# Kernel tuning notes

Measured on AMD Instinct MI355X. Metric: run time of the kernel, lower is better.

## Reference

```python
import jax, jax.numpy as jnp
import numpy as np

L = 5  # number of attention+MLP stages

def _layernorm(x, g, b, eps=1e-5):
    mu = x.mean(-1, keepdims=True)
    var = ((x - mu) ** 2).mean(-1, keepdims=True)
    return (x - mu) * jax.lax.rsqrt(var + eps) * g + b

def setup_inputs() -> dict:
    key = jax.random.key(0)
    B, N, C = 8, 2048, 512  # win_size=4, num_slices=12 -> C = 4*4*384//12 = 512
    ks = jax.random.split(key, 7)
    s = 0.02
    return {
        "x": jax.random.normal(ks[0], (B, N, C), dtype=jnp.float32),
        "qkv_w": jax.random.normal(ks[1], (L, C, 3 * C), dtype=jnp.float32) * s,
        "qkv_b": jnp.zeros((L, 3 * C), dtype=jnp.float32),
        "ln_g": jnp.ones((L, C), dtype=jnp.float32),
        "ln_b": jnp.zeros((L, C), dtype=jnp.float32),
        "fc1_w": jax.random.normal(ks[2], (L, C, 2 * C), dtype=jnp.float32) * s,
        "fc1_b": jnp.zeros((L, 2 * C), dtype=jnp.float32),
        "fc2_w": jax.random.normal(ks[3], (L, 2 * C, C), dtype=jnp.float32) * s,
        "fc2_b": jnp.zeros((L, C), dtype=jnp.float32),
    }

def reference(x, qkv_w, qkv_b, ln_g, ln_b, fc1_w, fc1_b, fc2_w, fc2_b):
    B, N, C = x.shape
    half = N // 2
    scale = C ** -0.5  # num_heads = 1 -> head_dim = C
    # Custom block mask: top-left (half x half) block fully visible,
    # top-right block masked; bottom half is tril with diagonal = N//2,
    # i.e. global row i >= half may attend to columns j <= i.
    i = jnp.arange(N)[:, None]
    j = jnp.arange(N)[None, :]
    allowed = jnp.where(i < half, j < half, j <= i)
    bias = jnp.where(allowed, 0.0, -1000.0).astype(x.dtype)  # (N, N)
    for l in range(L):
        # Mask3dAttention (single head)
        qkv = x @ qkv_w[l] + qkv_b[l]                      # (B, N, 3C)
        q, k, v = jnp.split(qkv, 3, axis=-1)               # each (B, N, C)
        attn = jnp.einsum("bnc,bmc->bnm", q * scale, k) + bias
        attn = jax.nn.softmax(attn, axis=-1)
        x = jnp.einsum("bnm,bmc->bnc", attn, v)
        # residual MLP on normed features
        y = _layernorm(x, ln_g[l], ln_b[l])
        h = jax.nn.gelu(y @ fc1_w[l] + fc1_b[l], approximate=False)
        x = x + (h @ fc2_w[l] + fc2_b[l])
    return x
```

## Files before the change

### kernel.cpp

```cpp
#include <hip/hip_runtime.h>
#include <math.h>

typedef unsigned short u16;
typedef __attribute__((ext_vector_type(8))) short bf16x8;
typedef __attribute__((ext_vector_type(4))) float f32x4;
typedef __attribute__((ext_vector_type(4))) unsigned short u16x4;

#define NLAYERS 5
#define BATCH 8
#define SEQ 2048
#define CH 512
#define ROWS_TOTAL (BATCH * SEQ)
#define HALF (SEQ / 2)
#define QSCALE_EXP2 0.06375871529f
#define EXP2_CAP 86.56f

#define SMEM_U16 32768
#define QK2_U16 32768

__device__ __forceinline__ u16 f2bf(float f) {
    unsigned u = __float_as_uint(f);
    u += 0x7fffu + ((u >> 16) & 1u);
    return (u16)(u >> 16);
}

__device__ __forceinline__ unsigned pk2(float a, float b) {
    unsigned r;
    asm("v_cvt_pk_bf16_f32 %0, %1, %2" : "=v"(r) : "v"(a), "v"(b));
    return r;
}

__device__ __forceinline__ u16x4 pack4(f32x4 v) {
    union { unsigned u[2]; u16x4 o; } r;
    r.u[0] = pk2(v[0], v[1]);
    r.u[1] = pk2(v[2], v[3]);
    return r.o;
}

__device__ __forceinline__ void st16(u16* p, u16x4 v) { *(u16x4*)p = v; }
__device__ __forceinline__ void st16f(float* p, f32x4 v) { *(f32x4*)p = v; }

__device__ __forceinline__ float fexp2(float x) {
    float r;
    asm("v_exp_f32 %0, %1" : "=v"(r) : "v"(x));
    return r;
}

__device__ __forceinline__ void llds16(const u16* g, u16* l) {
    __builtin_amdgcn_global_load_lds(
        (const __attribute__((address_space(1))) unsigned int*)g,
        (__attribute__((address_space(3))) unsigned int*)l, 16, 0, 0);
}

__device__ __forceinline__ void xcd_rc(int& rt, int& ct) {
    const int n = blockIdx.x;
    const int m = n >> 3;
    rt = (n & 7) * 16 + (m & 15);
    ct = m >> 4;
}

__device__ __forceinline__ void mm_compute(const u16* As, const u16* Bs,
                                           const int aoff[2][4],
                                           const int boff[2][4],
                                           f32x4 acc[4][4])
{
#pragma unroll
    for (int h = 0; h < 2; ++h) {
        bf16x8 af[4], bfv[4];
#pragma unroll
        for (int t = 0; t < 4; ++t) af[t]  = *(const bf16x8*)&As[aoff[h][t]];
#pragma unroll
        for (int t = 0; t < 4; ++t) bfv[t] = *(const bf16x8*)&Bs[boff[h][t]];
#pragma unroll
        for (int ti = 0; ti < 4; ++ti)
#pragma unroll
            for (int tj = 0; tj < 4; ++tj)
                acc[ti][tj] = __builtin_amdgcn_mfma_f32_16x16x32_bf16(
                    af[ti], bfv[tj], acc[ti][tj], 0, 0, 0);
    }
}

__device__ __forceinline__ void mm_issue(const u16* gA, const u16* gB,
                                         u16* lA, u16* lB, int lda, int ldb)
{
#pragma unroll
    for (int i = 0; i < 4; ++i)
        llds16(gA + (size_t)i * 32 * lda, lA + i * 2048);
#pragma unroll
    for (int i = 0; i < 4; ++i)
        llds16(gB + (size_t)i * 32 * ldb, lB + i * 2048);
}

__device__ __forceinline__ void mm_core(
    const u16* __restrict__ A, int lda,
    const u16* __restrict__ Bt, int ldb,
    int row0, int col0, int K,
    u16* SM, f32x4 acc[4][4])
{
    const int tid  = threadIdx.x;
    const int wave = tid >> 6, lane = tid & 63;
    const int wm = (wave & 1) * 64, wn = (wave >> 1) * 64;
    const int q  = lane >> 4,  ln = lane & 15;

    const int sr8 = lane >> 3;
    const int sc  = (lane & 7) ^ sr8;
    const u16* gA = A  + (size_t)(row0 + wave * 8 + sr8) * lda + sc * 8;
    const u16* gB = Bt + (size_t)(col0 + wave * 8 + sr8) * ldb + sc * 8;

    u16* const A0 = SM;
    u16* const B0 = SM + 8192;
    u16* const A1 = SM + 16384;
    u16* const B1 = SM + 24576;
    u16* const w0a = A0 + wave * 512;
    u16* const w0b = B0 + wave * 512;
    u16* const w1a = A1 + wave * 512;
    u16* const w1b = B1 + wave * 512;

    int aoff[2][4], boff[2][4];
#pragma unroll
    for (int h = 0; h < 2; ++h) {
        const int pos = (((h * 4 + q) ^ (ln & 7)) * 8);
#pragma unroll
        for (int t = 0; t < 4; ++t) {
            aoff[h][t] = (wm + t * 16 + ln) * 64 + pos;
            boff[h][t] = (wn + t * 16 + ln) * 64 + pos;
        }
    }

#pragma unroll
    for (int ti = 0; ti < 4; ++ti)
#pragma unroll
        for (int tj = 0; tj < 4; ++tj)
#pragma unroll
            for (int e = 0; e < 4; ++e) acc[ti][tj][e] = 0.f;

    mm_issue(gA, gB, w0a, w0b, lda, ldb);
    gA += 64; gB += 64;

    for (int k0 = 0; k0 < K; k0 += 128) {
        if (k0 + 64 < K) {
            mm_issue(gA, gB, w1a, w1b, lda, ldb);
            gA += 64; gB += 64;
            asm volatile("s_waitcnt vmcnt(8)" ::: "memory");
        } else {
            asm volatile("s_waitcnt vmcnt(0)" ::: "memory");
        }
        __builtin_amdgcn_s_barrier();
        mm_compute(A0, B0, aoff, boff, acc);
        __builtin_amdgcn_s_barrier();
        __builtin_amdgcn_sched_barrier(0);
        if (k0 + 128 < K) {
            mm_issue(gA, gB, w0a, w0b, lda, ldb);
            gA += 64; gB += 64;
            asm volatile("s_waitcnt vmcnt(8)" ::: "memory");
        } else {
            asm volatile("s_waitcnt vmcnt(0)" ::: "memory");
        }
        __builtin_amdgcn_s_barrier();
        mm_compute(A1, B1, aoff, boff, acc);
        __builtin_amdgcn_s_barrier();
        __builtin_amdgcn_sched_barrier(0);
    }
}

template <typename F>
__device__ __forceinline__ void epi_emit(f32x4 acc[4][4], float* eb, F emit)
{
    const int tid = threadIdx.x, wave = tid >> 6, lane = tid & 63;
    const int wn = (wave >> 1) * 64;
    const int q = lane >> 4, ln = lane & 15;
#pragma unroll
    for (int p = 0; p < 4; ++p) {
        __syncthreads();
        if ((wave & 1) == (p >> 1)) {
            const int tibase = (p & 1) * 2;
#pragma unroll
            for (int tj = 0; tj < 4; ++tj)
#pragma unroll
                for (int t2 = 0; t2 < 2; ++t2)
#pragma unroll
                    for (int r = 0; r < 4; ++r)
                        eb[(t2 * 16 + q * 4 + r) * 132 + wn + tj * 16 + ln] =
                            acc[tibase + t2][tj][r];
        }
        __syncthreads();
#pragma unroll
        for (int s = 0; s < 4; ++s) {
            const int row = s * 8 + (tid >> 5);
            const int col = (tid & 31) * 4;
            f32x4 v = *(const f32x4*)&eb[row * 132 + col];
            emit(p * 32 + row, col, v);
        }
    }
}

__global__ __launch_bounds__(256) void qkv_gemm(
    const u16* __restrict__ A, const u16* __restrict__ Bt,
    const float* __restrict__ bias,
    u16* __restrict__ Qb, u16* __restrict__ Kb, u16* __restrict__ Vt,
    float* __restrict__ rowsum)
{
    __shared__ __align__(16) u16 SMEM[SMEM_U16];
    f32x4 acc[4][4];
    int rt, ct; xcd_rc(rt, ct);
    const int row0 = rt * 128, col0 = ct * 128;
    if (ct == 0 && threadIdx.x < 128)
        rowsum[row0 + threadIdx.x] = 0.f;
    mm_core(A, CH, Bt, CH, row0, col0, CH, SMEM, acc);

    if (ct < 8) {
        u16* dst = (ct < 4) ? Qb : Kb;
        const int cbase = (ct < 4) ? col0 : col0 - CH;
        const float sc = (ct < 4) ? QSCALE_EXP2 : 1.0f;
        epi_emit(acc, (float*)SMEM, [&](int row, int col, f32x4 v) {
            const float4 bb = *(const float4*)&bias[col0 + col];
            v[0] = (v[0] + bb.x) * sc; v[1] = (v[1] + bb.y) * sc;
            v[2] = (v[2] + bb.z) * sc; v[3] = (v[3] + bb.w) * sc;
            st16(&dst[(size_t)(row0 + row) * CH + cbase + col], pack4(v));
        });
    } else {
        const int tid = threadIdx.x, wave = tid >> 6, lane = tid & 63;
        const int wm = (wave & 1) * 64, wn = (wave >> 1) * 64;
        const int q = lane >> 4, ln = lane & 15;
#pragma unroll
        for (int tj = 0; tj < 4; ++tj) {
            const int gcol = col0 + wn + tj * 16 + ln;
            const float bv = bias[gcol];
#pragma unroll
            for (int ti = 0; ti < 4; ++ti) {
                const int grow = row0 + wm + ti * 16 + q * 4;
                const int b = grow >> 11, j = grow & (SEQ - 1);
                f32x4 vv;
                vv[0] = acc[ti][tj][0] + bv; vv[1] = acc[ti][tj][1] + bv;
                vv[2] = acc[ti][tj][2] + bv; vv[3] = acc[ti][tj][3] + bv;
                st16(&Vt[(size_t)b * CH * SEQ +
                         (size_t)(gcol - 2 * CH) * SEQ + j], pack4(vv));
            }
        }
    }
}

__global__ __launch_bounds__(512, 4) void qk2_gemm(
    const u16* __restrict__ Qb, const u16* __restrict__ Kb,
    u16* __restrict__ Sb, float* __restrict__ rowsum)
{
    __shared__ __align__(16) u16 SMEM[QK2_U16];
    u16* const B0 = SMEM;
    u16* const B1 = SMEM + 16384;
    float* const eb = (float*)SMEM;

    const int id = blockIdx.x;
    const int b = id & 7;
    int u = id >> 3, it, pr;
    if (u < 32) { it = u >> 2; pr = u & 3; }
    else {
        int v = u - 32; it = 8; int len = 5;
        while (v >= len) { v -= len; ++it; len = 5 + ((it - 8) >> 1); }
        pr = v;
    }

    const int tid = threadIdx.x;
    const int w = tid >> 6, lane = tid & 63;
    const int wq = w & 3;
    const int wm = (wq & 1) * 64;
    const int wn = (w >> 2) * 128 + (wq >> 1) * 64;
    const int q = lane >> 4, ln = lane & 15;
    const int sr8 = lane >> 3, sc = (lane & 7) ^ sr8;

    const int row0 = it * 128, col0 = pr * 256;
    const u16* const Qg = Qb + (size_t)b * SEQ * CH;
    const u16* const Kg = Kb + (size_t)b * SEQ * CH;
    u16* const S = Sb + (size_t)b * SEQ * SEQ;

    const u16* gB = Kg + (size_t)(col0 + w * 32 + sr8) * CH + sc * 8;
    u16* const lB0 = B0 + w * 2048;
    u16* const lB1 = B1 + w * 2048;

    const u16* const gAf = Qg + (size_t)(row0 + wm + ln) * CH + q * 8;

    int boff[2][4];
#pragma unroll
    for (int h = 0; h < 2; ++h) {
        const int pos = (((h * 4 + q) ^ (ln & 7)) * 8);
#pragma unroll
        for (int t = 0; t < 4; ++t)
            boff[h][t] = (wn + t * 16 + ln) * 64 + pos;
    }

    f32x4 acc[4][4];
#pragma unroll
    for (int ti = 0; ti < 4; ++ti)
#pragma unroll
        for (int tj = 0; tj < 4; ++tj)
#pragma unroll
            for (int e = 0; e < 4; ++e) acc[ti][tj][e] = 0.f;

#pragma unroll
    for (int i = 0; i < 4; ++i)
        llds16(gB + (size_t)(i * 8) * CH, lB0 + i * 512);

    for (int s = 0; s < 8; ++s) {
        bf16x8 af[2][4];
#pragma unroll
        for (int h = 0; h < 2; ++h)
#pragma unroll
            for (int t = 0; t < 4; ++t)
                af[h][t] = *(const bf16x8*)(gAf + (size_t)(t * 16) * CH
                                            + s * 64 + h * 32);
        if (s < 7) {
            u16* const nb = (s & 1) ? lB0 : lB1;
#pragma unroll
            for (int i = 0; i < 4; ++i)
                llds16(gB + (size_t)(i * 8) * CH + (s + 1) * 64, nb + i * 512);
            asm volatile("s_waitcnt vmcnt(4)" ::: "memory");
        } else {
            asm volatile("s_waitcnt vmcnt(0)" ::: "memory");
        }
        __builtin_amdgcn_s_barrier();
        const u16* const Bc = (s & 1) ? B1 : B0;
#pragma unroll
        for (int h = 0; h < 2; ++h) {
            bf16x8 bfv[4];
#pragma unroll
            for (int t = 0; t < 4; ++t)
                bfv[t] = *(const bf16x8*)&Bc[boff[h][t]];
#pragma unroll
            for (int ti = 0; ti < 4; ++ti)
#pragma unroll
                for (int tj = 0; tj < 4; ++tj)
                    acc[ti][tj] = __builtin_amdgcn_mfma_f32_16x16x32_bf16(
                        af[h][ti], bfv[tj], acc[ti][tj], 0, 0, 0);
        }
        __builtin_amdgcn_s_barrier();
        __builtin_amdgcn_sched_barrier(0);
    }

    const bool upper = (it < 8);
#pragma unroll
    for (int p = 0; p < 4; ++p) {
        __syncthreads();
        if ((wq & 1) == (p >> 1)) {
            const int tibase = (p & 1) * 2;
#pragma unroll
            for (int tj = 0; tj < 4; ++tj)
#pragma unroll
                for (int t2 = 0; t2 < 2; ++t2)
#pragma unroll
                    for (int r = 0; r < 4; ++r)
                        eb[(t2 * 16 + q * 4 + r) * 260 + wn + tj * 16 + ln] =
                            acc[tibase + t2][tj][r];
        }
        __syncthreads();
#pragma unroll
        for (int s2 = 0; s2 < 4; ++s2) {
            const int row = s2 * 8 + w;
            const int col = lane * 4;
            f32x4 v = *(const f32x4*)&eb[row * 260 + col];
            const int grow = row0 + p * 32 + row;
            const int gcol = col0 + col;
            f32x4 pv;
#pragma unroll
            for (int e = 0; e < 4; ++e) {
                const bool allowed = upper || (gcol + e <= grow);
                pv[e] = allowed ? fexp2(fminf(v[e], EXP2_CAP)) : 0.f;
            }
            st16(&S[(size_t)grow * SEQ + gcol], pack4(pv));
            float rs = pv[0] + pv[1] + pv[2] + pv[3];
            rs += __shfl_xor(rs, 1, 64);
            rs += __shfl_xor(rs, 2, 64);
            rs += __shfl_xor(rs, 4, 64);
            rs += __shfl_xor(rs, 8, 64);
            rs += __shfl_xor(rs, 16, 64);
            rs += __shfl_xor(rs, 32, 64);
            if (lane == 0)
                atomicAdd(&rowsum[b * SEQ + grow], rs);
        }
    }
}

__global__ __launch_bounds__(256) void pv_gemm(
    const u16* __restrict__ Sb, const u16* __restrict__ Vt,
    const float* __restrict__ rowsum, float* __restrict__ O)
{
    const int n = blockIdx.x;
    const int b = n & 7, m = n >> 3;
    const int it = 15 - (m >> 2), ct = m & 3;
    const int Kfull = ((it < 8) ? 8 : (it + 1)) * 128;
    __shared__ __align__(16) u16 SMEM[SMEM_U16];
    f32x4 acc[4][4];
    const u16* A  = Sb + (size_t)b * SEQ * SEQ;
    const u16* Bt = Vt + (size_t)b * CH * SEQ;
    const int row0 = it * 128, col0 = ct * 128;
    mm_core(A, SEQ, Bt, SEQ, row0, col0, Kfull, SMEM, acc);

    epi_emit(acc, (float*)SMEM, [&](int row, int col, f32x4 v) {
        const int grow = row0 + row;
        const float rden = 1.0f / rowsum[b * SEQ + grow];
        v[0] *= rden; v[1] *= rden; v[2] *= rden; v[3] *= rden;
        st16f(&O[(size_t)(b * SEQ + grow) * CH + col0 + col], v);
    });
}

__global__ __launch_bounds__(256) void fc1_gemm(
    const u16* __restrict__ A, const u16* __restrict__ Bt,
    const float* __restrict__ bias, u16* __restrict__ H)
{
    __shared__ __align__(16) u16 SMEM[SMEM_U16];
    f32x4 acc[4][4];
    int rt, ct; xcd_rc(rt, ct);
    const int row0 = rt * 128, col0 = ct * 128;
    mm_core(A, CH, Bt, CH, row0, col0, CH, SMEM, acc);
    epi_emit(acc, (float*)SMEM, [&](int row, int col, f32x4 v) {
        const float4 bb = *(const float4*)&bias[col0 + col];
        v[0] += bb.x; v[1] += bb.y; v[2] += bb.z; v[3] += bb.w;
#pragma unroll
        for (int e = 0; e < 4; ++e)
            v[e] = 0.5f * v[e] * (1.f + erff(v[e] * 0.70710678118654752f));
        st16(&H[(size_t)(row0 + row) * (2 * CH) + col0 + col], pack4(v));
    });
}

template <bool WRITE_X>
__global__ __launch_bounds__(256) void fc2_gemm(
    const u16* __restrict__ A, const u16* __restrict__ Bt,
    const float* __restrict__ bias, float* __restrict__ X,
    u16* __restrict__ Xb)
{
    __shared__ __align__(16) u16 SMEM[SMEM_U16];
    f32x4 acc[4][4];
    int rt, ct; xcd_rc(rt, ct);
    const int row0 = rt * 128, col0 = ct * 128;
    mm_core(A, 2 * CH, Bt, 2 * CH, row0, col0, 2 * CH, SMEM, acc);
    epi_emit(acc, (float*)SMEM, [&](int row, int col, f32x4 v) {
        const size_t idx = (size_t)(row0 + row) * CH + col0 + col;
        const float4 bb = *(const float4*)&bias[col0 + col];
        const f32x4 xv = *(const f32x4*)&X[idx];
        v[0] += bb.x + xv[0]; v[1] += bb.y + xv[1];
        v[2] += bb.z + xv[2]; v[3] += bb.w + xv[3];
        if (WRITE_X) st16f(&X[idx], v);
        st16(&Xb[idx], pack4(v));
    });
}

__global__ __launch_bounds__(256) void ln_kernel(
    const float* __restrict__ x, const float* __restrict__ g,
    const float* __restrict__ bta, u16* __restrict__ y)
{
    const int tid = threadIdx.x, wave = tid >> 6, lane = tid & 63;
    const int row = (blockIdx.x & 7) * SEQ + (blockIdx.x >> 3) * 4 + wave;
    const size_t base = (size_t)row * CH + lane * 8;
    const float4 a = *(const float4*)&x[base];
    const float4 b = *(const float4*)&x[base + 4];
    float s = a.x + a.y + a.z + a.w + b.x + b.y + b.z + b.w;
#pragma unroll
    for (int off = 1; off < 64; off <<= 1) s += __shfl_xor(s, off, 64);
    const float mu = s * (1.f / CH);
    float d[8] = { a.x - mu, a.y - mu, a.z - mu, a.w - mu,
                   b.x - mu, b.y - mu, b.z - mu, b.w - mu };
    float ss = 0.f;
#pragma unroll
    for (int e = 0; e < 8; ++e) ss += d[e] * d[e];
#pragma unroll
    for (int off = 1; off < 64; off <<= 1) ss += __shfl_xor(ss, off, 64);
    const float w = 1.f / sqrtf(ss * (1.f / CH) + 1e-5f);
    const int c = lane * 8;
    const float4 g0 = *(const float4*)&g[c],   g1 = *(const float4*)&g[c + 4];
    const float4 t0 = *(const float4*)&bta[c], t1 = *(const float4*)&bta[c + 4];
    uint4 o;
    o.x = pk2(d[0] * w * g0.x + t0.x, d[1] * w * g0.y + t0.y);
    o.y = pk2(d[2] * w * g0.z + t0.z, d[3] * w * g0.w + t0.w);
    o.z = pk2(d[4] * w * g1.x + t1.x, d[5] * w * g1.y + t1.y);
    o.w = pk2(d[6] * w * g1.z + t1.z, d[7] * w * g1.w + t1.w);
    *(uint4*)&y[base] = o;
}

__global__ __launch_bounds__(256) void f2bf_kernel(
    const float* __restrict__ in, u16* __restrict__ out)
{
    const int i = blockIdx.x * 256 + threadIdx.x;
    float4 vv = ((const float4*)in)[i];
    f32x4 v; v[0] = vv.x; v[1] = vv.y; v[2] = vv.z; v[3] = vv.w;
    u16x4 o = pack4(v);
    *(u16x4*)&out[(size_t)i * 4] = o;
}

__global__ __launch_bounds__(256) void wtrans_kernel(
    const float* __restrict__ in, u16* __restrict__ out, int K, int N)
{
    __shared__ float tile[32][33];
    const int l = blockIdx.z;
    in  += (size_t)l * K * N;
    out += (size_t)l * K * N;
    const int n0 = blockIdx.x * 32, k0 = blockIdx.y * 32;
    const int r = threadIdx.x >> 3, c4 = (threadIdx.x & 7) * 4;
    float4 v = *(const float4*)&in[(size_t)(k0 + r) * N + n0 + c4];
    tile[r][c4 + 0] = v.x; tile[r][c4 + 1] = v.y;
    tile[r][c4 + 2] = v.z; tile[r][c4 + 3] = v.w;
    __syncthreads();
    f32x4 t;
    t[0] = tile[c4 + 0][r]; t[1] = tile[c4 + 1][r];
    t[2] = tile[c4 + 2][r]; t[3] = tile[c4 + 3][r];
    st16(&out[(size_t)(n0 + r) * K + k0 + c4], pack4(t));
}

extern "C" void kernel_launch(void* const* d_in, const int* in_sizes, int n_in,
                              void* d_out, int out_size, void* d_ws, size_t ws_size,
                              hipStream_t stream)
{
    const float* x_in  = (const float*)d_in[0];
    const float* qkv_w = (const float*)d_in[1];
    const float* qkv_b = (const float*)d_in[2];
    const float* ln_g  = (const float*)d_in[3];
    const float* ln_b  = (const float*)d_in[4];
    const float* fc1_w = (const float*)d_in[5];
    const float* fc1_b = (const float*)d_in[6];
    const float* fc2_w = (const float*)d_in[7];
    const float* fc2_b = (const float*)d_in[8];

    float* xbuf = (float*)d_out;

    char* p = (char*)d_ws;
    u16* qkv_wt = (u16*)p; p += (size_t)NLAYERS * 1536 * 512 * 2;
    u16* fc1_wt = (u16*)p; p += (size_t)NLAYERS * 1024 * 512 * 2;
    u16* fc2_wt = (u16*)p; p += (size_t)NLAYERS * 512 * 1024 * 2;
    u16* xb = (u16*)p; p += (size_t)ROWS_TOTAL * CH * 2;
    u16* Qb = (u16*)p; p += (size_t)ROWS_TOTAL * CH * 2;
    u16* Kb = (u16*)p; p += (size_t)ROWS_TOTAL * CH * 2;
    u16* Vt = (u16*)p; p += (size_t)ROWS_TOTAL * CH * 2;
    float* rowsum = (float*)p; p += (size_t)ROWS_TOTAL * 4;
    u16* Sb = (u16*)p;
    u16* yb = Sb;
    u16* hb = Sb + (size_t)ROWS_TOTAL * CH;

    const dim3 blk(256);
    const dim3 blk2(512);

    f2bf_kernel<<<dim3(ROWS_TOTAL * CH / 1024), blk, 0, stream>>>(x_in, xb);
    wtrans_kernel<<<dim3(1536 / 32, 512 / 32, NLAYERS), blk, 0, stream>>>(
        qkv_w, qkv_wt, 512, 1536);
    wtrans_kernel<<<dim3(1024 / 32, 512 / 32, NLAYERS), blk, 0, stream>>>(
        fc1_w, fc1_wt, 512, 1024);
    wtrans_kernel<<<dim3(512 / 32, 1024 / 32, NLAYERS), blk, 0, stream>>>(
        fc2_w, fc2_wt, 1024, 512);

    for (int l = 0; l < NLAYERS; ++l) {
        qkv_gemm<<<dim3(128 * 12), blk, 0, stream>>>(
            xb, qkv_wt + (size_t)l * 1536 * 512, qkv_b + (size_t)l * 1536,
            Qb, Kb, Vt, rowsum);
        qk2_gemm<<<dim3(672), blk2, 0, stream>>>(Qb, Kb, Sb, rowsum);
        pv_gemm<<<dim3(512), blk, 0, stream>>>(Sb, Vt, rowsum, xbuf);
        ln_kernel<<<dim3(ROWS_TOTAL / 4), blk, 0, stream>>>(
            xbuf, ln_g + (size_t)l * CH, ln_b + (size_t)l * CH, yb);
        fc1_gemm<<<dim3(128 * 8), blk, 0, stream>>>(
            yb, fc1_wt + (size_t)l * 1024 * 512, fc1_b + (size_t)l * 1024, hb);
        if (l < NLAYERS - 1)
            fc2_gemm<false><<<dim3(128 * 4), blk, 0, stream>>>(
                hb, fc2_wt + (size_t)l * 512 * 1024, fc2_b + (size_t)l * 512,
                xbuf, xb);
        else
            fc2_gemm<true><<<dim3(128 * 4), blk, 0, stream>>>(
                hb, fc2_wt + (size_t)l * 512 * 1024, fc2_b + (size_t)l * 512,
                xbuf, xb);
    }
}
```

Baseline: 1.117 ms.

## Stage Q tile through LDS and prefetch K two steps ahead in qk2_gemm

```diff
diff --git a/kernel.cpp b/kernel.cpp
--- a/kernel.cpp
+++ b/kernel.cpp
@@ -16,7 +16,7 @@
 #define EXP2_CAP 86.56f
 
 #define SMEM_U16 32768
-#define QK2_U16 32768
+#define QK2_U16 40960
 
 __device__ __forceinline__ u16 f2bf(float f) {
     unsigned u = __float_as_uint(f);
@@ -245,8 +245,9 @@
     u16* __restrict__ Sb, float* __restrict__ rowsum)
 {
     __shared__ __align__(16) u16 SMEM[QK2_U16];
-    u16* const B0 = SMEM;
-    u16* const B1 = SMEM + 16384;
+    u16* const As = SMEM;
+    u16* const B0 = SMEM + 8192;
+    u16* const B1 = SMEM + 24576;
     float* const eb = (float*)SMEM;
 
     const int id = blockIdx.x;
@@ -272,19 +273,21 @@
     const u16* const Kg = Kb + (size_t)b * SEQ * CH;
     u16* const S = Sb + (size_t)b * SEQ * SEQ;
 
+    const u16* gA = Qg + (size_t)(row0 + w * 16 + sr8) * CH + sc * 8;
+    u16* const lA = As + w * 1024;
     const u16* gB = Kg + (size_t)(col0 + w * 32 + sr8) * CH + sc * 8;
     u16* const lB0 = B0 + w * 2048;
     u16* const lB1 = B1 + w * 2048;
 
-    const u16* const gAf = Qg + (size_t)(row0 + wm + ln) * CH + q * 8;
-
-    int boff[2][4];
+    int aoff[2][4], boff[2][4];
 #pragma unroll
     for (int h = 0; h < 2; ++h) {
         const int pos = (((h * 4 + q) ^ (ln & 7)) * 8);
 #pragma unroll
-        for (int t = 0; t < 4; ++t)
+        for (int t = 0; t < 4; ++t) {
+            aoff[h][t] = (wm + t * 16 + ln) * 64 + pos;
             boff[h][t] = (wn + t * 16 + ln) * 64 + pos;
+        }
     }
 
     f32x4 acc[4][4];
@@ -298,41 +301,32 @@
 #pragma unroll
     for (int i = 0; i < 4; ++i)
         llds16(gB + (size_t)(i * 8) * CH, lB0 + i * 512);
+    llds16(gA,                  lA);
+    llds16(gA + (size_t)8 * CH, lA + 512);
+#pragma unroll
+    for (int i = 0; i < 4; ++i)
+        llds16(gB + (size_t)(i * 8) * CH + 64, lB1 + i * 512);
 
     for (int s = 0; s < 8; ++s) {
-        bf16x8 af[2][4];
-#pragma unroll
-        for (int h = 0; h < 2; ++h)
-#pragma unroll
-            for (int t = 0; t < 4; ++t)
-                af[h][t] = *(const bf16x8*)(gAf + (size_t)(t * 16) * CH
-                                            + s * 64 + h * 32);
-        if (s < 7) {
-            u16* const nb = (s & 1) ? lB0 : lB1;
-#pragma unroll
-            for (int i = 0; i < 4; ++i)
-                llds16(gB + (size_t)(i * 8) * CH + (s + 1) * 64, nb + i * 512);
+        if (s < 7)
             asm volatile("s_waitcnt vmcnt(4)" ::: "memory");
-        } else {
+        else
             asm volatile("s_waitcnt vmcnt(0)" ::: "memory");
-        }
         __builtin_amdgcn_s_barrier();
-        const u16* const Bc = (s & 1) ? B1 : B0;
-#pragma unroll
-        for (int h = 0; h < 2; ++h) {
-            bf16x8 bfv[4];
-#pragma unroll
-            for (int t = 0; t < 4; ++t)
-                bfv[t] = *(const bf16x8*)&Bc[boff[h][t]];
-#pragma unroll
-            for (int ti = 0; ti < 4; ++ti)
-#pragma unroll
-                for (int tj = 0; tj < 4; ++tj)
-                    acc[ti][tj] = __builtin_amdgcn_mfma_f32_16x16x32_bf16(
-                        af[h][ti], bfv[tj], acc[ti][tj], 0, 0, 0);
-        }
+        mm_compute(As, (s & 1) ? B1 : B0, aoff, boff, acc);
         __builtin_amdgcn_s_barrier();
         __builtin_amdgcn_sched_barrier(0);
+        if (s < 7) {
+            llds16(gA + (s + 1) * 64,                    lA);
+            llds16(gA + (s + 1) * 64 + (size_t)8 * CH,   lA + 512);
+            if (s < 6) {
+                u16* const nb = (s & 1) ? lB1 : lB0;
+#pragma unroll
+                for (int i = 0; i < 4; ++i)
+                    llds16(gB + (size_t)(i * 8) * CH + (s + 2) * 64,
+                           nb + i * 512);
+            }
+        }
     }
 
     const bool upper = (it < 8);
```

Result: faster. 939.5 us (-15.9%).
